# Kernel tuning notes

Measured on AMD Instinct MI355X. Metric: run time of the kernel, lower is better.

## Reference

```python
import jax, jax.numpy as jnp
import numpy as np

# Grid of blocks: blocks[i][j] is Linear(D, D) if mask[i, j] else None.
N_OUT, N_IN, D, B = 8, 8, 128, 32768
BAND = 2  # active blocks: j <= i and i - j <= BAND


def setup_inputs() -> dict:
    key = jax.random.key(0)
    k1, k2, k3 = jax.random.split(key, 3)
    # X: (num input blocks, batch, block feature dim)
    X = jax.random.normal(k1, (N_IN, B, D), dtype=jnp.float32)
    # W[i, j]: torch.nn.Linear weight of block (i, j), shape (out, in)
    W = jax.random.normal(k2, (N_OUT, N_IN, D, D), dtype=jnp.float32) / np.sqrt(D).astype(np.float32)
    b = jax.random.normal(k3, (N_OUT, N_IN, D), dtype=jnp.float32) * 0.01
    i = jnp.arange(N_OUT)[:, None]
    j = jnp.arange(N_IN)[None, :]
    mask = (j <= i) & (i - j <= BAND)  # banded lower-triangular block sparsity
    return {"X": X, "W": W, "b": b, "mask": mask}


def reference(X, W, b, mask):
    # Sequential2D forward: out[i] = sum_j (X[j] @ W[i,j].T + b[i,j]) over active blocks.
    # None blocks contribute a zero vector, which we express by zeroing masked weights/biases.
    m = mask.astype(W.dtype)                       # (i, j)
    Wm = W * m[:, :, None, None]                   # zero out None blocks
    out = jnp.einsum('jbd,ijod->ibo', X, Wm)       # block-row summation of Linear outputs
    bias = jnp.sum(b * m[:, :, None], axis=1)      # (i, o): sum of active biases per row
    return out + bias[:, None, :]                  # (num_out_blocks, batch, block_out)
```

## Files before the change

### kernel.cpp

```cpp
#include <hip/hip_runtime.h>
#include <hip/hip_bf16.h>


#define NOUT  8
#define NIN   8
#define DD    128
#define BATCH 32768
#define BAND  2

#define BM 128
#define BN 128
#define BK 64
#define SK (BK + 8)

typedef __attribute__((ext_vector_type(8))) short  short8;
typedef __attribute__((ext_vector_type(4))) float  floatx4;

__device__ __forceinline__ unsigned short f2bf(float f) {
    unsigned int u = __float_as_uint(f);
    u += 0x7fffu + ((u >> 16) & 1u);
    return (unsigned short)(u >> 16);
}

__device__ __forceinline__ short8 pack8(floatx4 f0, floatx4 f1) {
    short8 p;
    p[0] = (short)f2bf(f0[0]); p[1] = (short)f2bf(f0[1]);
    p[2] = (short)f2bf(f0[2]); p[3] = (short)f2bf(f0[3]);
    p[4] = (short)f2bf(f1[0]); p[5] = (short)f2bf(f1[1]);
    p[6] = (short)f2bf(f1[2]); p[7] = (short)f2bf(f1[3]);
    return p;
}

__global__ __launch_bounds__(512)
void seq2d_kernel(const float* __restrict__ X,
                  const float* __restrict__ W,
                  const float* __restrict__ Bv,
                  float* __restrict__ out) {
    const int i  = blockIdx.y;
    const int m0 = blockIdx.x * BM;

    __shared__ unsigned short sA[BM * SK];
    __shared__ unsigned short sB[BN * SK];
    __shared__ float sbias[DD];

    const int tid  = threadIdx.x;
    const int lane = tid & 63;
    const int wave = tid >> 6;
    const int wm   = (wave & 1) * 64;
    const int wn   = (wave >> 1) * 32;
    const int l15  = lane & 15;
    const int quad = lane >> 4;

    int jlo = i - BAND; if (jlo < 0) jlo = 0;
    const int nc = (i - jlo + 1) * 2;

    if (tid < DD) {
        float s = 0.f;
        for (int j = jlo; j <= i; ++j)
            s += Bv[(i * NIN + j) * DD + tid];
        sbias[tid] = s;
    }

    floatx4 acc[4][2];
#pragma unroll
    for (int a = 0; a < 4; ++a)
#pragma unroll
        for (int c = 0; c < 2; ++c)
            acc[a][c] = (floatx4){0.f, 0.f, 0.f, 0.f};

    const int srow = tid >> 3;
    const int scol = (tid & 7) << 3;

    floatx4 pa[4], pb[4];

    auto prefetch = [&](int c) {
        const int j  = jlo + (c >> 1);
        const int k0 = (c & 1) * BK;
        const float* __restrict__ xa =
            X + (size_t)j * BATCH * DD + (size_t)(m0 + srow) * DD + k0 + scol;
        pa[0] = *(const floatx4*)(xa);
        pa[1] = *(const floatx4*)(xa + 4);
        pa[2] = *(const floatx4*)(xa + 64 * DD);
        pa[3] = *(const floatx4*)(xa + 64 * DD + 4);
        const float* __restrict__ wb =
            W + (size_t)(i * NIN + j) * DD * DD + (size_t)srow * DD + k0 + scol;
        pb[0] = *(const floatx4*)(wb);
        pb[1] = *(const floatx4*)(wb + 4);
        pb[2] = *(const floatx4*)(wb + 64 * DD);
        pb[3] = *(const floatx4*)(wb + 64 * DD + 4);
    };

    prefetch(0);

    for (int c = 0; c < nc; ++c) {
        __syncthreads();
        *(short8*)(&sA[srow * SK + scol])        = pack8(pa[0], pa[1]);
        *(short8*)(&sA[(64 + srow) * SK + scol]) = pack8(pa[2], pa[3]);
        *(short8*)(&sB[srow * SK + scol])        = pack8(pb[0], pb[1]);
        *(short8*)(&sB[(64 + srow) * SK + scol]) = pack8(pb[2], pb[3]);
        if (c + 1 < nc) prefetch(c + 1);
        __syncthreads();

#pragma unroll
        for (int kk = 0; kk < BK; kk += 32) {
            short8 af[4], bfr[2];
#pragma unroll
            for (int t = 0; t < 4; ++t)
                af[t] = *(const short8*)(&sA[(wm + t * 16 + l15) * SK + kk + quad * 8]);
#pragma unroll
            for (int t = 0; t < 2; ++t)
                bfr[t] = *(const short8*)(&sB[(wn + t * 16 + l15) * SK + kk + quad * 8]);
#pragma unroll
            for (int mt = 0; mt < 4; ++mt)
#pragma unroll
                for (int nt = 0; nt < 2; ++nt)
                    acc[mt][nt] = __builtin_amdgcn_mfma_f32_16x16x32_bf16(
                        af[mt], bfr[nt], acc[mt][nt], 0, 0, 0);
        }
    }

    float* outi = out + (size_t)i * BATCH * DD;
#pragma unroll
    for (int mt = 0; mt < 4; ++mt) {
#pragma unroll
        for (int nt = 0; nt < 2; ++nt) {
            const int n_g  = wn + nt * 16 + l15;
            const float bs = sbias[n_g];
            const int m_b  = m0 + wm + mt * 16 + quad * 4;
#pragma unroll
            for (int r = 0; r < 4; ++r)
                outi[(size_t)(m_b + r) * DD + n_g] = acc[mt][nt][r] + bs;
        }
    }
}

extern "C" void kernel_launch(void* const* d_in, const int* in_sizes, int n_in,
                              void* d_out, int out_size, void* d_ws, size_t ws_size,
                              hipStream_t stream) {
    const float* X  = (const float*)d_in[0];
    const float* W  = (const float*)d_in[1];
    const float* Bv = (const float*)d_in[2];
    float* out = (float*)d_out;

    dim3 grid(BATCH / BM, NOUT);
    seq2d_kernel<<<grid, 512, 0, stream>>>(X, W, Bv, out);
}
```

Before: 262.3 us.

## Double-buffer LDS tiles, use packed bf16 conversion, and remap load lanes

Switches to two LDS buffers so the next chunk is staged after the MFMA loop, which leaves one barrier per iteration instead of two. Uses the hardware packed bf16 convert builtin when it is available. Remaps each thread to load 16 contiguous floats of one row, and raises the launch bounds occupancy hint to 4. The cost is doubled LDS use, about 74KB per block, which limits how many blocks fit per CU.

Result: no change. 266.6 us (+1.6%).

```diff
diff --git a/kernel.cpp b/kernel.cpp
--- a/kernel.cpp
+++ b/kernel.cpp
@@ -12,9 +12,11 @@
 #define BN 128
 #define BK 64
 #define SK (BK + 8)
+#define BUFE (BM * SK)
 
-typedef __attribute__((ext_vector_type(8))) short  short8;
-typedef __attribute__((ext_vector_type(4))) float  floatx4;
+typedef __attribute__((ext_vector_type(8))) short        short8;
+typedef __attribute__((ext_vector_type(4))) float        floatx4;
+typedef __attribute__((ext_vector_type(4))) unsigned int uint4v;
 
 __device__ __forceinline__ unsigned short f2bf(float f) {
     unsigned int u = __float_as_uint(f);
@@ -22,16 +24,17 @@
     return (unsigned short)(u >> 16);
 }
 
-__device__ __forceinline__ short8 pack8(floatx4 f0, floatx4 f1) {
-    short8 p;
-    p[0] = (short)f2bf(f0[0]); p[1] = (short)f2bf(f0[1]);
-    p[2] = (short)f2bf(f0[2]); p[3] = (short)f2bf(f0[3]);
-    p[4] = (short)f2bf(f1[0]); p[5] = (short)f2bf(f1[1]);
-    p[6] = (short)f2bf(f1[2]); p[7] = (short)f2bf(f1[3]);
-    return p;
+__device__ __forceinline__ unsigned int pk2(float lo, float hi) {
+#if __has_builtin(__builtin_amdgcn_cvt_pk_bf16_f32)
+    typedef __attribute__((ext_vector_type(2))) __bf16 bf16x2_t;
+    bf16x2_t v = __builtin_amdgcn_cvt_pk_bf16_f32(lo, hi);
+    return __builtin_bit_cast(unsigned int, v);
+#else
+    return ((unsigned int)f2bf(hi) << 16) | (unsigned int)f2bf(lo);
+#endif
 }
 
-__global__ __launch_bounds__(512)
+__global__ __launch_bounds__(512, 4)
 void seq2d_kernel(const float* __restrict__ X,
                   const float* __restrict__ W,
                   const float* __restrict__ Bv,
@@ -39,8 +42,7 @@
     const int i  = blockIdx.y;
     const int m0 = blockIdx.x * BM;
 
-    __shared__ unsigned short sA[BM * SK];
-    __shared__ unsigned short sB[BN * SK];
+    __shared__ unsigned short sAll[4 * BUFE];
     __shared__ float sbias[DD];
 
     const int tid  = threadIdx.x;
@@ -68,48 +70,59 @@
         for (int c = 0; c < 2; ++c)
             acc[a][c] = (floatx4){0.f, 0.f, 0.f, 0.f};
 
-    const int srow = tid >> 3;
-    const int scol = (tid & 7) << 3;
+    const int srow = tid >> 2;
+    const int scol = (tid & 3) << 4;
+    const size_t xrow_off = (size_t)(m0 + srow) * DD + scol;
+    const size_t wrow_off = (size_t)srow * DD + scol;
 
     floatx4 pa[4], pb[4];
 
     auto prefetch = [&](int c) {
         const int j  = jlo + (c >> 1);
         const int k0 = (c & 1) * BK;
-        const float* __restrict__ xa =
-            X + (size_t)j * BATCH * DD + (size_t)(m0 + srow) * DD + k0 + scol;
-        pa[0] = *(const floatx4*)(xa);
-        pa[1] = *(const floatx4*)(xa + 4);
-        pa[2] = *(const floatx4*)(xa + 64 * DD);
-        pa[3] = *(const floatx4*)(xa + 64 * DD + 4);
-        const float* __restrict__ wb =
-            W + (size_t)(i * NIN + j) * DD * DD + (size_t)srow * DD + k0 + scol;
-        pb[0] = *(const floatx4*)(wb);
-        pb[1] = *(const floatx4*)(wb + 4);
-        pb[2] = *(const floatx4*)(wb + 64 * DD);
-        pb[3] = *(const floatx4*)(wb + 64 * DD + 4);
+        const float* __restrict__ xa = X + (size_t)j * BATCH * DD + xrow_off + k0;
+#pragma unroll
+        for (int t = 0; t < 4; ++t) pa[t] = *(const floatx4*)(xa + t * 4);
+        const float* __restrict__ wb = W + (size_t)(i * NIN + j) * DD * DD + wrow_off + k0;
+#pragma unroll
+        for (int t = 0; t < 4; ++t) pb[t] = *(const floatx4*)(wb + t * 4);
+    };
+
+    auto stage = [&](int buf) {
+        unsigned short* dA = sAll + buf * (2 * BUFE);
+        uint4v a0 = (uint4v){pk2(pa[0][0], pa[0][1]), pk2(pa[0][2], pa[0][3]),
+                             pk2(pa[1][0], pa[1][1]), pk2(pa[1][2], pa[1][3])};
+        uint4v a1 = (uint4v){pk2(pa[2][0], pa[2][1]), pk2(pa[2][2], pa[2][3]),
+                             pk2(pa[3][0], pa[3][1]), pk2(pa[3][2], pa[3][3])};
+        uint4v b0 = (uint4v){pk2(pb[0][0], pb[0][1]), pk2(pb[0][2], pb[0][3]),
+                             pk2(pb[1][0], pb[1][1]), pk2(pb[1][2], pb[1][3])};
+        uint4v b1 = (uint4v){pk2(pb[2][0], pb[2][1]), pk2(pb[2][2], pb[2][3]),
+                             pk2(pb[3][0], pb[3][1]), pk2(pb[3][2], pb[3][3])};
+        *(uint4v*)(&dA[srow * SK + scol])            = a0;
+        *(uint4v*)(&dA[srow * SK + scol + 8])        = a1;
+        *(uint4v*)(&dA[BUFE + srow * SK + scol])     = b0;
+        *(uint4v*)(&dA[BUFE + srow * SK + scol + 8]) = b1;
     };
 
     prefetch(0);
+    stage(0);
 
     for (int c = 0; c < nc; ++c) {
         __syncthreads();
-        *(short8*)(&sA[srow * SK + scol])        = pack8(pa[0], pa[1]);
-        *(short8*)(&sA[(64 + srow) * SK + scol]) = pack8(pa[2], pa[3]);
-        *(short8*)(&sB[srow * SK + scol])        = pack8(pb[0], pb[1]);
-        *(short8*)(&sB[(64 + srow) * SK + scol]) = pack8(pb[2], pb[3]);
-        if (c + 1 < nc) prefetch(c + 1);
-        __syncthreads();
+        const bool more = (c + 1 < nc);
+        if (more) prefetch(c + 1);
 
+        const unsigned short* bA = sAll + (c & 1) * (2 * BUFE);
+        const unsigned short* bB = bA + BUFE;
 #pragma unroll
         for (int kk = 0; kk < BK; kk += 32) {
             short8 af[4], bfr[2];
 #pragma unroll
             for (int t = 0; t < 4; ++t)
-                af[t] = *(const short8*)(&sA[(wm + t * 16 + l15) * SK + kk + quad * 8]);
+                af[t] = *(const short8*)(&bA[(wm + t * 16 + l15) * SK + kk + quad * 8]);
 #pragma unroll
             for (int t = 0; t < 2; ++t)
-                bfr[t] = *(const short8*)(&sB[(wn + t * 16 + l15) * SK + kk + quad * 8]);
+                bfr[t] = *(const short8*)(&bB[(wn + t * 16 + l15) * SK + kk + quad * 8]);
 #pragma unroll
             for (int mt = 0; mt < 4; ++mt)
 #pragma unroll
@@ -117,6 +130,8 @@
                     acc[mt][nt] = __builtin_amdgcn_mfma_f32_16x16x32_bf16(
                         af[mt], bfr[nt], acc[mt][nt], 0, 0, 0);
         }
+
+        if (more) stage((c + 1) & 1);
     }
 
     float* outi = out + (size_t)i * BATCH * DD;
```
